# Optimization experiments

Measured on AMD Instinct MI355X. Metric: run time of the kernel, lower is better.

## Reference

```python
import jax, jax.numpy as jnp
import numpy as np

N_NODES = 50000
N_EDGES = 800000
N_GRAPHS = 64
IN_CH = 128
HID_G = 256
HID_FC = 256
OUT_CH = 128


def setup_inputs() -> dict:
    key = jax.random.key(0)
    ks = jax.random.split(key, 16)
    x = jax.random.normal(ks[0], (N_NODES, IN_CH), dtype=jnp.float32)
    edge_index = jax.random.randint(ks[1], (2, N_EDGES), 0, N_NODES, dtype=jnp.int64)
    batch = jnp.sort(jax.random.randint(ks[2], (N_NODES,), 0, N_GRAPHS, dtype=jnp.int64))
    hlr = jax.random.normal(ks[3], (N_GRAPHS, 1), dtype=jnp.float32)
    std = jax.random.normal(ks[4], (N_GRAPHS, 1), dtype=jnp.float32)
    s = 0.05
    W0 = jax.random.normal(ks[5], (IN_CH, HID_G), dtype=jnp.float32) * s
    b0 = jnp.zeros((HID_G,), jnp.float32)
    W1 = jax.random.normal(ks[6], (HID_G, HID_G), dtype=jnp.float32) * s
    b1 = jnp.zeros((HID_G,), jnp.float32)
    W2 = jax.random.normal(ks[7], (HID_G, HID_G), dtype=jnp.float32) * s
    b2 = jnp.zeros((HID_G,), jnp.float32)
    fcW0 = jax.random.normal(ks[8], (HID_G + 2, HID_FC), dtype=jnp.float32) * s
    fcb0 = jnp.zeros((HID_FC,), jnp.float32)
    fcW1 = jax.random.normal(ks[9], (HID_FC, OUT_CH), dtype=jnp.float32) * s
    fcb1 = jnp.zeros((OUT_CH,), jnp.float32)
    return dict(x=x, edge_index=edge_index, batch=batch, hlr=hlr, std=std,
                W0=W0, b0=b0, W1=W1, b1=b1, W2=W2, b2=b2,
                fcW0=fcW0, fcb0=fcb0, fcW1=fcW1, fcb1=fcb1)


def _gcn_conv(h, W, b, src, dst, dis):
    # GCNConv with added self-loops and symmetric normalization:
    # out_i = sum_{j->i} d_j^{-1/2} d_i^{-1/2} (h_j W) + d_i^{-1} (h_i W) + b
    hW = h @ W  # [N, F]
    norm = dis[src] * dis[dst]  # [E]
    agg = jax.ops.segment_sum(hW[src] * norm[:, None], dst, num_segments=N_NODES)
    agg = agg + hW * (dis * dis)[:, None]  # self-loop contribution
    return agg + b


def reference(x, edge_index, batch, hlr, std, W0, b0, W1, b1, W2, b2, fcW0, fcb0, fcW1, fcb1):
    src, dst = edge_index[0], edge_index[1]
    # degree on A + I (edge weight 1), computed at destination nodes
    deg = jax.ops.segment_sum(jnp.ones((N_EDGES,), x.dtype), dst, num_segments=N_NODES) + 1.0
    dis = jax.lax.rsqrt(deg)
    h = jax.nn.relu(_gcn_conv(x, W0, b0, src, dst, dis))
    h = jax.nn.relu(_gcn_conv(h, W1, b1, src, dst, dis))
    h = jax.nn.relu(_gcn_conv(h, W2, b2, src, dst, dis))
    # global mean pool over graphs
    counts = jax.ops.segment_sum(jnp.ones((N_NODES,), x.dtype), batch, num_segments=N_GRAPHS)
    pooled = jax.ops.segment_sum(h, batch, num_segments=N_GRAPHS) / jnp.maximum(counts, 1.0)[:, None]
    z = jnp.concatenate([pooled, hlr, std], axis=1)  # [G, HID_G + 2]
    z = jax.nn.relu(z @ fcW0 + fcb0)
    return z @ fcW1 + fcb1
```

## Files before the change

kernel.cpp:

```cpp
#include <hip/hip_runtime.h>

#define NNODES 50000
#define NEDGES 800000
#define NGRAPHS 64
#define INCH 128
#define HID 256
#define ZSTR (HID + 2)
#define SCAN_B 512
#define SCAN_NB ((NNODES + SCAN_B - 1) / SCAN_B)
#define NSLICE 16
#define FILL_PASSES 4
#define PASS_NODES ((NNODES + FILL_PASSES - 1) / FILL_PASSES)

typedef __attribute__((ext_vector_type(8))) short short8v;
typedef __attribute__((ext_vector_type(8))) unsigned short ushort8v;
typedef __attribute__((ext_vector_type(4))) float f32x4;

__device__ inline ushort f2b(float f) {
    union { float f; unsigned u; } v; v.f = f;
    unsigned r = (v.u + 0x7FFFu + ((v.u >> 16) & 1u)) >> 16;
    return (ushort)r;
}
__device__ inline float b2f(ushort b) {
    union { unsigned u; float f; } v; v.u = ((unsigned)b) << 16;
    return v.f;
}

__global__ __launch_bounds__(256) void fill_pre(const int* __restrict__ dst, int* __restrict__ deg,
                                                int* __restrict__ pwn) {
    int e = blockIdx.x * 256 + threadIdx.x;
    if (e < NEDGES) pwn[e] = atomicAdd(&deg[dst[e]], 1);
}

__global__ __launch_bounds__(256) void dis_kernel(const int* __restrict__ deg, float* __restrict__ dis) {
    int i = blockIdx.x * 256 + threadIdx.x;
    if (i < NNODES) dis[i] = rsqrtf((float)deg[i] + 1.0f);
}

__global__ __launch_bounds__(SCAN_B) void scan1(const int* __restrict__ deg, int* __restrict__ row_ptr,
                                                int* __restrict__ bsum) {
    __shared__ int s[SCAN_B];
    int t = threadIdx.x;
    int i = blockIdx.x * SCAN_B + t;
    int v = (i < NNODES) ? deg[i] : 0;
    s[t] = v;
    __syncthreads();
    for (int off = 1; off < SCAN_B; off <<= 1) {
        int x = (t >= off) ? s[t - off] : 0;
        __syncthreads();
        if (t >= off) s[t] += x;
        __syncthreads();
    }
    if (i < NNODES) row_ptr[i + 1] = s[t];
    if (t == SCAN_B - 1) bsum[blockIdx.x] = s[t];
}

__global__ __launch_bounds__(128) void scan2(int* __restrict__ bsum) {
    __shared__ int s[128];
    int t = threadIdx.x;
    int v = (t < SCAN_NB) ? bsum[t] : 0;
    s[t] = v;
    __syncthreads();
    for (int off = 1; off < 128; off <<= 1) {
        int x = (t >= off) ? s[t - off] : 0;
        __syncthreads();
        if (t >= off) s[t] += x;
        __syncthreads();
    }
    if (t < SCAN_NB) bsum[t] = s[t];
}

__global__ __launch_bounds__(SCAN_B) void scan3(int* __restrict__ row_ptr, const int* __restrict__ bsum) {
    int b = blockIdx.x, t = threadIdx.x;
    int i = b * SCAN_B + t;
    if (i == 0) row_ptr[0] = 0;
    if (i < NNODES && b > 0) row_ptr[i + 1] += bsum[b - 1];
}

__global__ __launch_bounds__(256) void fill_scatter(const int* __restrict__ src, const int* __restrict__ dst,
                                                    const int* __restrict__ pwn, const int* __restrict__ row_ptr,
                                                    int* __restrict__ csr_src, int lo) {
    int e = blockIdx.x * 256 + threadIdx.x;
    if (e >= NEDGES) return;
    int d = dst[e];
    if (d < lo || d >= lo + PASS_NODES) return;
    csr_src[row_ptr[d] + pwn[e]] = src[e];
}

__global__ __launch_bounds__(256) void xcvt(const float4* __restrict__ x, const float* __restrict__ dis,
                                            ushort4* __restrict__ xb, int n4) {
    int i = blockIdx.x * 256 + threadIdx.x;
    if (i >= n4) return;
    float d = dis[i >> 5];
    float4 v = x[i];
    ushort4 o;
    o.x = f2b(d * v.x); o.y = f2b(d * v.y); o.z = f2b(d * v.z); o.w = f2b(d * v.w);
    xb[i] = o;
}

__global__ __launch_bounds__(256) void wcvt(const float* __restrict__ W, ushort* __restrict__ Wt, int K, int N) {
    int i = blockIdx.x * 256 + threadIdx.x;
    if (i >= K * N) return;
    int k = i / N, n = i - k * N;
    Wt[n * K + k] = f2b(W[i]);
}

template <int K>
__global__ __launch_bounds__(512, 4) void gcn_fused(const ushort* __restrict__ hin,
                                                    const int* __restrict__ row_ptr,
                                                    const int* __restrict__ csr_src,
                                                    const ushort* __restrict__ Bt,
                                                    const float* __restrict__ bias,
                                                    const float* __restrict__ dis,
                                                    ushort* __restrict__ hout, int scale_out) {
    __shared__ ushort As[128 * K];
    const int tid = threadIdx.x;
    const int w = tid >> 6, l = tid & 63;
    const int R0 = blockIdx.x * 128;

    constexpr int CHL = K / 8;
    constexpr int NPW = 64 / CHL;
    const int sub = l / CHL;
    const int lane = l - sub * CHL;
    const ushort* hp = hin + lane * 8;
#pragma unroll
    for (int it = 0; it < 128 / (8 * NPW); ++it) {
        int nloc = (it * 8 + w) * NPW + sub;
        int node = R0 + nloc;
        if (node < NNODES) {
            ushort8v sv = *(const ushort8v*)&hp[(size_t)node * K];
            float a0 = b2f(sv[0]), a1 = b2f(sv[1]), a2 = b2f(sv[2]), a3 = b2f(sv[3]);
            float a4 = b2f(sv[4]), a5 = b2f(sv[5]), a6 = b2f(sv[6]), a7 = b2f(sv[7]);
            int e = row_ptr[node], e1 = row_ptr[node + 1];
            for (; e + 7 < e1; e += 8) {
                ushort8v v[8];
#pragma unroll
                for (int u = 0; u < 8; ++u) v[u] = *(const ushort8v*)&hp[(size_t)csr_src[e + u] * K];
#pragma unroll
                for (int u = 0; u < 8; ++u) {
                    a0 += b2f(v[u][0]); a1 += b2f(v[u][1]); a2 += b2f(v[u][2]); a3 += b2f(v[u][3]);
                    a4 += b2f(v[u][4]); a5 += b2f(v[u][5]); a6 += b2f(v[u][6]); a7 += b2f(v[u][7]);
                }
            }
            for (; e < e1; ++e) {
                ushort8v v0 = *(const ushort8v*)&hp[(size_t)csr_src[e] * K];
                a0 += b2f(v0[0]); a1 += b2f(v0[1]); a2 += b2f(v0[2]); a3 += b2f(v0[3]);
                a4 += b2f(v0[4]); a5 += b2f(v0[5]); a6 += b2f(v0[6]); a7 += b2f(v0[7]);
            }
            ushort8v o;
            o[0] = f2b(a0); o[1] = f2b(a1); o[2] = f2b(a2); o[3] = f2b(a3);
            o[4] = f2b(a4); o[5] = f2b(a5); o[6] = f2b(a6); o[7] = f2b(a7);
            *(ushort8v*)&As[nloc * K + ((lane * 8) ^ ((nloc & 7) * 8))] = o;
        }
    }
    __syncthreads();

    const int wr = w >> 2, wc = w & 3;
    const int r16 = l & 15, kg = l >> 4;
    f32x4 acc[4][4] = {};
#pragma unroll
    for (int k0 = 0; k0 < K; k0 += 32) {
        int k = k0 + kg * 8;
        short8v a[4], b[4];
#pragma unroll
        for (int m = 0; m < 4; ++m) {
            int row = wr * 64 + m * 16 + r16;
            a[m] = *(const short8v*)&As[row * K + (k ^ ((row & 7) * 8))];
        }
#pragma unroll
        for (int n = 0; n < 4; ++n)
            b[n] = *(const short8v*)&Bt[(size_t)(wc * 64 + n * 16 + r16) * K + k];
#pragma unroll
        for (int m = 0; m < 4; ++m)
#pragma unroll
            for (int n = 0; n < 4; ++n)
                acc[m][n] = __builtin_amdgcn_mfma_f32_16x16x32_bf16(a[m], b[n], acc[m][n], 0, 0, 0);
    }
    float bv[4];
#pragma unroll
    for (int n = 0; n < 4; ++n) bv[n] = bias[wc * 64 + n * 16 + r16];
#pragma unroll
    for (int m = 0; m < 4; ++m) {
#pragma unroll
        for (int j = 0; j < 4; ++j) {
            int row = R0 + wr * 64 + m * 16 + kg * 4 + j;
            if (row >= NNODES) continue;
            float dr = dis[row];
            float os = scale_out ? dr : 1.0f;
#pragma unroll
            for (int n = 0; n < 4; ++n) {
                float v = fmaxf(dr * acc[m][n][j] + bv[n], 0.f) * os;
                hout[(size_t)row * HID + wc * 64 + n * 16 + r16] = f2b(v);
            }
        }
    }
}

__global__ __launch_bounds__(256) void graph_bounds(const int* __restrict__ batch, int* __restrict__ gstart) {
    int i = blockIdx.x * 256 + threadIdx.x;
    if (i >= NNODES) return;
    int b = batch[i];
    if (i == 0) {
        for (int g = 0; g <= b; ++g) gstart[g] = 0;
    } else {
        int pb = batch[i - 1];
        for (int g = pb + 1; g <= b; ++g) gstart[g] = i;
    }
    if (i == NNODES - 1) {
        for (int g = b + 1; g <= NGRAPHS; ++g) gstart[g] = NNODES;
    }
}

__global__ __launch_bounds__(HID) void pool_partial(const ushort* __restrict__ h, const int* __restrict__ gstart,
                                                    float* __restrict__ z) {
    int g = blockIdx.x;
    int s = blockIdx.y;
    int t = threadIdx.x;
    int n0 = gstart[g], n1 = gstart[g + 1];
    int cnt = n1 - n0;
    if (cnt <= 0) return;
    int len = (cnt + NSLICE - 1) / NSLICE;
    int a = n0 + s * len;
    int b = a + len < n1 ? a + len : n1;
    if (a >= b) return;
    float acc = 0.f;
    for (int n = a; n < b; ++n) acc += b2f(h[(size_t)n * HID + t]);
    atomicAdd(&z[g * ZSTR + t], acc);
}

__global__ __launch_bounds__(HID) void pool_finalize(const int* __restrict__ gstart, const float* __restrict__ hlr,
                                                     const float* __restrict__ stdv, float* __restrict__ z) {
    int g = blockIdx.x;
    int t = threadIdx.x;
    int cnt = gstart[g + 1] - gstart[g];
    float inv = 1.f / (float)(cnt > 0 ? cnt : 1);
    z[g * ZSTR + t] *= inv;
    if (t == 0) {
        z[g * ZSTR + HID] = hlr[g];
        z[g * ZSTR + HID + 1] = stdv[g];
    }
}

__global__ __launch_bounds__(HID) void fc_k(const float* __restrict__ z, const float* __restrict__ fcW0,
                                            const float* __restrict__ fcb0, const float* __restrict__ fcW1,
                                            const float* __restrict__ fcb1, float* __restrict__ out) {
    __shared__ float zs[ZSTR];
    __shared__ float z2[HID];
    int g = blockIdx.x;
    int t = threadIdx.x;
    zs[t] = z[g * ZSTR + t];
    if (t < 2) zs[HID + t] = z[g * ZSTR + HID + t];
    __syncthreads();
    float acc = fcb0[t];
    for (int k = 0; k < ZSTR; ++k) acc += zs[k] * fcW0[k * HID + t];
    z2[t] = fmaxf(acc, 0.f);
    __syncthreads();
    if (t < INCH) {
        float acc2 = fcb1[t];
        for (int k = 0; k < HID; ++k) acc2 += z2[k] * fcW1[k * INCH + t];
        out[g * INCH + t] = acc2;
    }
}

extern "C" void kernel_launch(void* const* d_in, const int* in_sizes, int n_in,
                              void* d_out, int out_size, void* d_ws, size_t ws_size,
                              hipStream_t stream) {
    const float* x = (const float*)d_in[0];
    const int* ei = (const int*)d_in[1];
    const int* src = ei;
    const int* dst = ei + NEDGES;
    const int* batch = (const int*)d_in[2];
    const float* hlr = (const float*)d_in[3];
    const float* stdv = (const float*)d_in[4];
    const float* W0 = (const float*)d_in[5];
    const float* b0 = (const float*)d_in[6];
    const float* W1 = (const float*)d_in[7];
    const float* b1 = (const float*)d_in[8];
    const float* W2 = (const float*)d_in[9];
    const float* b2 = (const float*)d_in[10];
    const float* fcW0 = (const float*)d_in[11];
    const float* fcb0 = (const float*)d_in[12];
    const float* fcW1 = (const float*)d_in[13];
    const float* fcb1 = (const float*)d_in[14];
    float* out = (float*)d_out;

    char* p = (char*)d_ws;
    auto alloc = [&](size_t bytes) -> char* {
        char* r = p;
        p += (bytes + 255) & ~(size_t)255;
        return r;
    };
    ushort* xb = (ushort*)alloc(sizeof(ushort) * (size_t)NNODES * INCH);
    ushort* h = (ushort*)alloc(sizeof(ushort) * (size_t)NNODES * HID);
    ushort* hb = (ushort*)alloc(sizeof(ushort) * (size_t)NNODES * HID);
    ushort* Wt0 = (ushort*)alloc(sizeof(ushort) * HID * INCH);
    ushort* Wt1 = (ushort*)alloc(sizeof(ushort) * HID * HID);
    ushort* Wt2 = (ushort*)alloc(sizeof(ushort) * HID * HID);
    float* dis = (float*)alloc(sizeof(float) * NNODES);
    int* deg = (int*)alloc(sizeof(int) * NNODES);
    int* row_ptr = (int*)alloc(sizeof(int) * (NNODES + 1));
    int* pwn = (int*)alloc(sizeof(int) * NEDGES);
    int* csr_src = (int*)alloc(sizeof(int) * NEDGES);
    int* bsum = (int*)alloc(sizeof(int) * 128);
    int* gstart = (int*)alloc(sizeof(int) * (NGRAPHS + 1));
    float* z = (float*)alloc(sizeof(float) * NGRAPHS * ZSTR);
    (void)ws_size; (void)in_sizes; (void)n_in; (void)out_size;

    const int eblocks = (NEDGES + 255) / 256;

    hipMemsetAsync(deg, 0, sizeof(int) * NNODES, stream);
    fill_pre<<<eblocks, 256, 0, stream>>>(dst, deg, pwn);
    dis_kernel<<<(NNODES + 255) / 256, 256, 0, stream>>>(deg, dis);
    scan1<<<SCAN_NB, SCAN_B, 0, stream>>>(deg, row_ptr, bsum);
    scan2<<<1, 128, 0, stream>>>(bsum);
    scan3<<<SCAN_NB, SCAN_B, 0, stream>>>(row_ptr, bsum);
    for (int pass = 0; pass < FILL_PASSES; ++pass)
        fill_scatter<<<eblocks, 256, 0, stream>>>(src, dst, pwn, row_ptr, csr_src, pass * PASS_NODES);

    xcvt<<<(NNODES * INCH / 4 + 255) / 256, 256, 0, stream>>>((const float4*)x, dis, (ushort4*)xb,
                                                              NNODES * INCH / 4);
    wcvt<<<(INCH * HID + 255) / 256, 256, 0, stream>>>(W0, Wt0, INCH, HID);
    wcvt<<<(HID * HID + 255) / 256, 256, 0, stream>>>(W1, Wt1, HID, HID);
    wcvt<<<(HID * HID + 255) / 256, 256, 0, stream>>>(W2, Wt2, HID, HID);

    const int gblocks = (NNODES + 127) / 128;
    gcn_fused<INCH><<<gblocks, 512, 0, stream>>>(xb, row_ptr, csr_src, Wt0, b0, dis, h, 1);
    gcn_fused<HID><<<gblocks, 512, 0, stream>>>(h, row_ptr, csr_src, Wt1, b1, dis, hb, 1);
    gcn_fused<HID><<<gblocks, 512, 0, stream>>>(hb, row_ptr, csr_src, Wt2, b2, dis, h, 0);

    graph_bounds<<<(NNODES + 255) / 256, 256, 0, stream>>>(batch, gstart);
    hipMemsetAsync(z, 0, sizeof(float) * NGRAPHS * ZSTR, stream);
    dim3 pgrid(NGRAPHS, NSLICE);
    pool_partial<<<pgrid, HID, 0, stream>>>(h, gstart, z);
    pool_finalize<<<NGRAPHS, HID, 0, stream>>>(gstart, hlr, stdv, z);
    fc_k<<<NGRAPHS, HID, 0, stream>>>(z, fcW0, fcb0, fcW1, fcb1, out);
}
```

Before: 341.1 us.

## Split fused GCN layer into column-sliced gather and separate MFMA GEMM

Replaces the fused gather-then-GEMM kernel with two kernels per layer. The first gathers neighbour features in 32-column slices into a global bf16 buffer, with slice as the fastest block index so concurrent blocks touch a narrower feature range and get better cache locality. The second is a standalone MFMA GEMM that reads A directly from global memory instead of LDS. The fill scatter also drops from 4 to 2 passes. This trades an extra global write and read of the aggregated matrix per layer, plus an unswizzled GEMM A-load path, for a more cache-friendly gather and higher occupancy without the large LDS tile.

```diff
diff --git a/kernel.cpp b/kernel.cpp
--- a/kernel.cpp
+++ b/kernel.cpp
@@ -9,7 +9,7 @@
 #define SCAN_B 512
 #define SCAN_NB ((NNODES + SCAN_B - 1) / SCAN_B)
 #define NSLICE 16
-#define FILL_PASSES 4
+#define FILL_PASSES 2
 #define PASS_NODES ((NNODES + FILL_PASSES - 1) / FILL_PASSES)
 
 typedef __attribute__((ext_vector_type(8))) short short8v;
@@ -105,71 +105,66 @@
     Wt[n * K + k] = f2b(W[i]);
 }
 
-template <int K>
-__global__ __launch_bounds__(512, 4) void gcn_fused(const ushort* __restrict__ hin,
+template <int K, int NSL>
+__global__ __launch_bounds__(256) void gather_slice(const ushort* __restrict__ hin,
                                                     const int* __restrict__ row_ptr,
                                                     const int* __restrict__ csr_src,
-                                                    const ushort* __restrict__ Bt,
-                                                    const float* __restrict__ bias,
-                                                    const float* __restrict__ dis,
-                                                    ushort* __restrict__ hout, int scale_out) {
-    __shared__ ushort As[128 * K];
+                                                    ushort* __restrict__ agg) {
+    const int s = blockIdx.x % NSL;
+    const int nb = blockIdx.x / NSL;
+    const int node = nb * 64 + (threadIdx.x >> 2);
+    if (node >= NNODES) return;
+    const int lane = threadIdx.x & 3;
+    const ushort* hp = hin + s * 32 + lane * 8;
+    ushort8v sv = *(const ushort8v*)&hp[(size_t)node * K];
+    float a0 = b2f(sv[0]), a1 = b2f(sv[1]), a2 = b2f(sv[2]), a3 = b2f(sv[3]);
+    float a4 = b2f(sv[4]), a5 = b2f(sv[5]), a6 = b2f(sv[6]), a7 = b2f(sv[7]);
+    int e = row_ptr[node], e1 = row_ptr[node + 1];
+    for (; e + 7 < e1; e += 8) {
+        ushort8v v[8];
+#pragma unroll
+        for (int u = 0; u < 8; ++u) v[u] = *(const ushort8v*)&hp[(size_t)csr_src[e + u] * K];
+#pragma unroll
+        for (int u = 0; u < 8; ++u) {
+            a0 += b2f(v[u][0]); a1 += b2f(v[u][1]); a2 += b2f(v[u][2]); a3 += b2f(v[u][3]);
+            a4 += b2f(v[u][4]); a5 += b2f(v[u][5]); a6 += b2f(v[u][6]); a7 += b2f(v[u][7]);
+        }
+    }
+    for (; e < e1; ++e) {
+        ushort8v v0 = *(const ushort8v*)&hp[(size_t)csr_src[e] * K];
+        a0 += b2f(v0[0]); a1 += b2f(v0[1]); a2 += b2f(v0[2]); a3 += b2f(v0[3]);
+        a4 += b2f(v0[4]); a5 += b2f(v0[5]); a6 += b2f(v0[6]); a7 += b2f(v0[7]);
+    }
+    ushort8v o;
+    o[0] = f2b(a0); o[1] = f2b(a1); o[2] = f2b(a2); o[3] = f2b(a3);
+    o[4] = f2b(a4); o[5] = f2b(a5); o[6] = f2b(a6); o[7] = f2b(a7);
+    *(ushort8v*)&agg[(size_t)node * K + s * 32 + lane * 8] = o;
+}
+
+__global__ __launch_bounds__(512) void gemm_mfma(const ushort* __restrict__ A, const ushort* __restrict__ Bt,
+                                                 const float* __restrict__ bias, const float* __restrict__ dis,
+                                                 ushort* __restrict__ C, int M, int K, int scale_out) {
     const int tid = threadIdx.x;
     const int w = tid >> 6, l = tid & 63;
-    const int R0 = blockIdx.x * 128;
-
-    constexpr int CHL = K / 8;
-    constexpr int NPW = 64 / CHL;
-    const int sub = l / CHL;
-    const int lane = l - sub * CHL;
-    const ushort* hp = hin + lane * 8;
-#pragma unroll
-    for (int it = 0; it < 128 / (8 * NPW); ++it) {
-        int nloc = (it * 8 + w) * NPW + sub;
-        int node = R0 + nloc;
-        if (node < NNODES) {
-            ushort8v sv = *(const ushort8v*)&hp[(size_t)node * K];
-            float a0 = b2f(sv[0]), a1 = b2f(sv[1]), a2 = b2f(sv[2]), a3 = b2f(sv[3]);
-            float a4 = b2f(sv[4]), a5 = b2f(sv[5]), a6 = b2f(sv[6]), a7 = b2f(sv[7]);
-            int e = row_ptr[node], e1 = row_ptr[node + 1];
-            for (; e + 7 < e1; e += 8) {
-                ushort8v v[8];
-#pragma unroll
-                for (int u = 0; u < 8; ++u) v[u] = *(const ushort8v*)&hp[(size_t)csr_src[e + u] * K];
-#pragma unroll
-                for (int u = 0; u < 8; ++u) {
-                    a0 += b2f(v[u][0]); a1 += b2f(v[u][1]); a2 += b2f(v[u][2]); a3 += b2f(v[u][3]);
-                    a4 += b2f(v[u][4]); a5 += b2f(v[u][5]); a6 += b2f(v[u][6]); a7 += b2f(v[u][7]);
-                }
-            }
-            for (; e < e1; ++e) {
-                ushort8v v0 = *(const ushort8v*)&hp[(size_t)csr_src[e] * K];
-                a0 += b2f(v0[0]); a1 += b2f(v0[1]); a2 += b2f(v0[2]); a3 += b2f(v0[3]);
-                a4 += b2f(v0[4]); a5 += b2f(v0[5]); a6 += b2f(v0[6]); a7 += b2f(v0[7]);
-            }
-            ushort8v o;
-            o[0] = f2b(a0); o[1] = f2b(a1); o[2] = f2b(a2); o[3] = f2b(a3);
-            o[4] = f2b(a4); o[5] = f2b(a5); o[6] = f2b(a6); o[7] = f2b(a7);
-            *(ushort8v*)&As[nloc * K + ((lane * 8) ^ ((nloc & 7) * 8))] = o;
-        }
-    }
-    __syncthreads();
-
     const int wr = w >> 2, wc = w & 3;
     const int r16 = l & 15, kg = l >> 4;
+    const int R = blockIdx.x * 128 + wr * 64;
+    const int Cb = wc * 64;
     f32x4 acc[4][4] = {};
-#pragma unroll
     for (int k0 = 0; k0 < K; k0 += 32) {
         int k = k0 + kg * 8;
         short8v a[4], b[4];
 #pragma unroll
         for (int m = 0; m < 4; ++m) {
-            int row = wr * 64 + m * 16 + r16;
-            a[m] = *(const short8v*)&As[row * K + (k ^ ((row & 7) * 8))];
+            int row = R + m * 16 + r16;
+            if (row > M - 1) row = M - 1;
+            a[m] = *(const short8v*)&A[(size_t)row * K + k];
         }
 #pragma unroll
-        for (int n = 0; n < 4; ++n)
-            b[n] = *(const short8v*)&Bt[(size_t)(wc * 64 + n * 16 + r16) * K + k];
+        for (int n = 0; n < 4; ++n) {
+            int col = Cb + n * 16 + r16;
+            b[n] = *(const short8v*)&Bt[(size_t)col * K + k];
+        }
 #pragma unroll
         for (int m = 0; m < 4; ++m)
 #pragma unroll
@@ -178,19 +173,19 @@
     }
     float bv[4];
 #pragma unroll
-    for (int n = 0; n < 4; ++n) bv[n] = bias[wc * 64 + n * 16 + r16];
+    for (int n = 0; n < 4; ++n) bv[n] = bias[Cb + n * 16 + r16];
 #pragma unroll
     for (int m = 0; m < 4; ++m) {
 #pragma unroll
         for (int j = 0; j < 4; ++j) {
-            int row = R0 + wr * 64 + m * 16 + kg * 4 + j;
-            if (row >= NNODES) continue;
+            int row = R + m * 16 + kg * 4 + j;
+            if (row >= M) continue;
             float dr = dis[row];
             float os = scale_out ? dr : 1.0f;
 #pragma unroll
             for (int n = 0; n < 4; ++n) {
                 float v = fmaxf(dr * acc[m][n][j] + bv[n], 0.f) * os;
-                hout[(size_t)row * HID + wc * 64 + n * 16 + r16] = f2b(v);
+                C[(size_t)row * HID + Cb + n * 16 + r16] = f2b(v);
             }
         }
     }
@@ -291,8 +286,8 @@
         return r;
     };
     ushort* xb = (ushort*)alloc(sizeof(ushort) * (size_t)NNODES * INCH);
+    ushort* agg = (ushort*)alloc(sizeof(ushort) * (size_t)NNODES * HID);
     ushort* h = (ushort*)alloc(sizeof(ushort) * (size_t)NNODES * HID);
-    ushort* hb = (ushort*)alloc(sizeof(ushort) * (size_t)NNODES * HID);
     ushort* Wt0 = (ushort*)alloc(sizeof(ushort) * HID * INCH);
     ushort* Wt1 = (ushort*)alloc(sizeof(ushort) * HID * HID);
     ushort* Wt2 = (ushort*)alloc(sizeof(ushort) * HID * HID);
@@ -323,10 +318,14 @@
     wcvt<<<(HID * HID + 255) / 256, 256, 0, stream>>>(W1, Wt1, HID, HID);
     wcvt<<<(HID * HID + 255) / 256, 256, 0, stream>>>(W2, Wt2, HID, HID);
 
+    const int nb64 = (NNODES + 63) / 64;
     const int gblocks = (NNODES + 127) / 128;
-    gcn_fused<INCH><<<gblocks, 512, 0, stream>>>(xb, row_ptr, csr_src, Wt0, b0, dis, h, 1);
-    gcn_fused<HID><<<gblocks, 512, 0, stream>>>(h, row_ptr, csr_src, Wt1, b1, dis, hb, 1);
-    gcn_fused<HID><<<gblocks, 512, 0, stream>>>(hb, row_ptr, csr_src, Wt2, b2, dis, h, 0);
+    gather_slice<INCH, 4><<<nb64 * 4, 256, 0, stream>>>(xb, row_ptr, csr_src, agg);
+    gemm_mfma<<<gblocks, 512, 0, stream>>>(agg, Wt0, b0, dis, h, NNODES, INCH, 1);
+    gather_slice<HID, 8><<<nb64 * 8, 256, 0, stream>>>(h, row_ptr, csr_src, agg);
+    gemm_mfma<<<gblocks, 512, 0, stream>>>(agg, Wt1, b1, dis, h, NNODES, HID, 1);
+    gather_slice<HID, 8><<<nb64 * 8, 256, 0, stream>>>(h, row_ptr, csr_src, agg);
+    gemm_mfma<<<gblocks, 512, 0, stream>>>(agg, Wt2, b2, dis, h, NNODES, HID, 0);
 
     graph_bounds<<<(NNODES + 255) / 256, 256, 0, stream>>>(batch, gstart);
     hipMemsetAsync(z, 0, sizeof(float) * NGRAPHS * ZSTR, stream);
```

After: 424.8 us. 1.25x slower.
